# Kernel tuning notes

Hardware: AMD Instinct MI355X
Metric: run time of the kernel (lower is better)

The kernel has to match this reference:

```python
import jax, jax.numpy as jnp
import numpy as np

N, E, G = 100000, 1600000, 512
D_IN, D_H, D_OUT = 128, 128, 1
EPS = 1e-5


def _gcn_conv(x, W, b, src, dst, n):
    # PyG GCNConv: h = x @ W, add self-loops, symmetric-normalized sum aggregation, bias after.
    h = x @ W
    loop = jnp.arange(n)
    s = jnp.concatenate([src, loop])
    d = jnp.concatenate([dst, loop])
    deg = jax.ops.segment_sum(jnp.ones(s.shape[0], dtype=h.dtype), d, num_segments=n)
    dinv = jnp.where(deg > 0, jax.lax.rsqrt(deg), 0.0)
    norm = dinv[s] * dinv[d]  # [E+N]
    out = jax.ops.segment_sum(h[s] * norm[:, None], d, num_segments=n)
    return out + b


def _bn(x, g, b, m, v):
    # eval-mode BatchNorm1d
    return (x - m) * jax.lax.rsqrt(v + EPS) * g + b


def setup_inputs() -> dict:
    key = jax.random.key(0)
    ks = jax.random.split(key, 24)
    x = jax.random.normal(ks[0], (N, D_IN), dtype=jnp.float32)
    edge_index = jax.random.randint(ks[1], (2, E), 0, N, dtype=jnp.int64)
    batch = (jnp.arange(N, dtype=jnp.int64) * G) // N  # sorted, all graphs non-empty
    inp = {"x": x, "edge_index": edge_index, "batch": batch}
    dims = [(D_IN, D_H), (D_H, D_H), (D_H, D_H)]
    for i, (din, dout) in enumerate(dims):
        sc = 1.0 / np.sqrt(din)
        inp[f"W{i}"] = jax.random.normal(ks[2 + 4 * i], (din, dout), dtype=jnp.float32) * sc
        inp[f"cb{i}"] = jnp.zeros((dout,), dtype=jnp.float32)
        inp[f"g{i}"] = jnp.ones((dout,), dtype=jnp.float32)
        inp[f"bt{i}"] = jnp.zeros((dout,), dtype=jnp.float32)
        inp[f"m{i}"] = jax.random.normal(ks[3 + 4 * i], (dout,), dtype=jnp.float32) * 0.1
        inp[f"v{i}"] = jax.random.uniform(ks[4 + 4 * i], (dout,), dtype=jnp.float32, minval=0.5, maxval=1.5)
    inp["L1w"] = jax.random.normal(ks[15], (2 * D_H, D_H), dtype=jnp.float32) / np.sqrt(2 * D_H)
    inp["L1b"] = jnp.zeros((D_H,), dtype=jnp.float32)
    inp["L2w"] = jax.random.normal(ks[16], (D_H, D_H // 2), dtype=jnp.float32) / np.sqrt(D_H)
    inp["L2b"] = jnp.zeros((D_H // 2,), dtype=jnp.float32)
    inp["L3w"] = jax.random.normal(ks[17], (D_H // 2, D_OUT), dtype=jnp.float32) / np.sqrt(D_H // 2)
    inp["L3b"] = jnp.zeros((D_OUT,), dtype=jnp.float32)
    return inp


def reference(x, edge_index, batch,
              W0, cb0, g0, bt0, m0, v0,
              W1, cb1, g1, bt1, m1, v1,
              W2, cb2, g2, bt2, m2, v2,
              L1w, L1b, L2w, L2b, L3w, L3b):
    src, dst = edge_index[0], edge_index[1]
    Ws = [W0, W1, W2]
    cbs = [cb0, cb1, cb2]
    bns = [(g0, bt0, m0, v0), (g1, bt1, m1, v1), (g2, bt2, m2, v2)]
    for i in range(3):
        x_prev = x
        x = _gcn_conv(x, Ws[i], cbs[i], src, dst, N)
        x = jax.nn.relu(_bn(x, *bns[i]))
        # dropout is identity in eval mode
        if i > 0:
            x = x + x_prev  # residual (shapes match for i > 0)
    ones = jnp.ones((N,), dtype=x.dtype)
    cnt = jax.ops.segment_sum(ones, batch, num_segments=G)[:, None]
    x_mean = jax.ops.segment_sum(x, batch, num_segments=G) / cnt
    x_max = jax.ops.segment_max(x, batch, num_segments=G)
    h = jnp.concatenate([x_mean, x_max], axis=1)  # [G, 2*D_H]
    h = jax.nn.relu(h @ L1w + L1b)
    h = jax.nn.relu(h @ L2w + L2b)
    return h @ L3w + L3b  # [G, 1]
```

## Files before the change

### kernel.cpp

```cpp
#include <hip/hip_runtime.h>
#include <math.h>

#define DH 128
#define EPSB 1e-5f
#define MAXB 832
#define BCAP 2560
#define LDAP 136

typedef __attribute__((ext_vector_type(8))) short short8;
typedef __attribute__((ext_vector_type(4))) float f32x4;

static __device__ __forceinline__ unsigned short f2bf(float f) {
    unsigned u = __float_as_uint(f);
    u += 0x7fffu + ((u >> 16) & 1u);
    return (unsigned short)(u >> 16);
}
static __device__ __forceinline__ float bf2f(unsigned short h) {
    return __uint_as_float(((unsigned)h) << 16);
}
static __device__ __forceinline__ float blo(unsigned u) { return __uint_as_float(u << 16); }
static __device__ __forceinline__ float bhi(unsigned u) { return __uint_as_float(u & 0xFFFF0000u); }


__launch_bounds__(256)
__global__ void k_bucketA(const int* __restrict__ src, const int* __restrict__ dst,
                          int* __restrict__ gcur, int* __restrict__ bbuf,
                          const int* __restrict__ batch, int* __restrict__ starts,
                          const float* __restrict__ W0, const float* __restrict__ W1,
                          const float* __restrict__ W2, unsigned short* __restrict__ Wf0,
                          int E, int NB, int chunk, int N, int G)
{
    const int t = threadIdx.x;

    if (blockIdx.x >= 512) {
        int fid = (blockIdx.x - 512) * 4 + (t >> 6);
        int lane = t & 63;
        int l = fid >> 6, f = fid & 63;
        const float* W = (l == 0) ? W0 : (l == 1) ? W1 : W2;
        unsigned short* Wf = Wf0 + (size_t)l * 32768;
        int nt = f & 3, s = (f >> 2) & 3, p = (f >> 4) & 1, nh = f >> 5;
        int n = nh * 64 + nt * 16 + (lane & 15);
        int kbase = s * 32 + (lane >> 4) * 8;
        unsigned short o[8];
#pragma unroll
        for (int j = 0; j < 8; ++j) {
            float w = W[(size_t)(kbase + j) * DH + n];
            unsigned short h = f2bf(w);
            o[j] = p ? f2bf(w - bf2f(h)) : h;
        }
        unsigned short* d = Wf + (size_t)f * 512 + lane * 8;
        *(ushort4*)d       = make_ushort4(o[0], o[1], o[2], o[3]);
        *(ushort4*)(d + 4) = make_ushort4(o[4], o[5], o[6], o[7]);
        return;
    }

    __shared__ int cnt[MAXB];
    __shared__ int base[MAXB];

    for (int i = blockIdx.x * 256 + t; i < N; i += 512 * 256) {
        int b = batch[i];
        if (i == 0) { starts[0] = 0; starts[G] = N; }
        else if (batch[i - 1] != b) starts[b] = i;
    }

    for (int i = t; i < NB; i += 256) cnt[i] = 0;
    __syncthreads();
    const int e0 = blockIdx.x * chunk;
    const int e1 = min(E, e0 + chunk);
    for (int e = e0 + t; e < e1; e += 256)
        atomicAdd(&cnt[dst[e] >> 7], 1);
    __syncthreads();
    for (int i = t; i < NB; i += 256) {
        int c = cnt[i];
        base[i] = (c > 0) ? atomicAdd(&gcur[i], c) : 0;
        cnt[i] = 0;
    }
    __syncthreads();
    for (int e = e0 + t; e < e1; e += 256) {
        int d = dst[e];
        int b = d >> 7;
        int o = base[b] + atomicAdd(&cnt[b], 1);
        if (o < BCAP) bbuf[(size_t)b * BCAP + o] = (src[e] << 7) | (d & 127);
    }
}


__launch_bounds__(256)
__global__ void k_bfinal(const int* __restrict__ gcur, int* __restrict__ bbuf,
                         int2* __restrict__ rowinfo, float* __restrict__ dinv, int N)
{
    __shared__ int ebuf[BCAP];
    __shared__ int dcnt[128];
    __shared__ int sp[128];
    const int b = blockIdx.x, t = threadIdx.x;
    const int c = min(gcur[b], BCAP);
    const int base = b * BCAP;
    int* p = bbuf + base;
    for (int i = t; i < c; i += 256) ebuf[i] = p[i];
    if (t < 128) dcnt[t] = 0;
    __syncthreads();
    for (int i = t; i < c; i += 256) atomicAdd(&dcnt[ebuf[i] & 127], 1);
    __syncthreads();
    if (t < 128) sp[t] = dcnt[t];
    __syncthreads();
    for (int off = 1; off < 128; off <<= 1) {
        int u = (t < 128 && t >= off) ? sp[t - off] : 0;
        __syncthreads();
        if (t < 128) sp[t] += u;
        __syncthreads();
    }
    if (t < 128) {
        sp[t] -= dcnt[t];
        int d = b * 128 + t;
        if (d < N) {
            rowinfo[d] = make_int2(base + sp[t], base + sp[t] + dcnt[t]);
            dinv[d] = rsqrtf((float)(dcnt[t] + 1));
        }
        dcnt[t] = 0;
    }
    __syncthreads();
    for (int i = t; i < c; i += 256) {
        int e = ebuf[i];
        int dl = e & 127;
        int o = atomicAdd(&dcnt[dl], 1);
        p[sp[dl] + o] = e >> 7;
    }
}


#define LDA0 132

__launch_bounds__(256)
__global__ void k_gemm0(const float* __restrict__ X,
                        const unsigned short* __restrict__ Wf,
                        const float* __restrict__ dinv,
                        unsigned short* __restrict__ hs, int N)
{
    __shared__ float As[64 * LDA0];

    const int tid  = threadIdx.x;
    const int lane = tid & 63, wave = tid >> 6;
    const int mh = wave >> 1, nh = wave & 1;
    const int rowBase = blockIdx.x * 64;
    const int r15 = lane & 15, quad = lane >> 4;

    {
        const float4* gp = (const float4*)(X + (size_t)rowBase * DH);
#pragma unroll
        for (int it = 0; it < 8; ++it) {
            int idx = it * 256 + tid;
            int grow = idx >> 5, gcol = idx & 31;
            float4 v = make_float4(0.f, 0.f, 0.f, 0.f);
            if (rowBase + grow < N) v = gp[idx];
            *(float4*)(As + grow * LDA0 + gcol * 4) = v;
        }
    }
    __syncthreads();

    f32x4 acc[2][4];
#pragma unroll
    for (int mt = 0; mt < 2; ++mt)
#pragma unroll
        for (int nt = 0; nt < 4; ++nt)
            acc[mt][nt] = (f32x4){0.f, 0.f, 0.f, 0.f};

#pragma unroll
    for (int s = 0; s < 4; ++s) {
        short8 wfh[4], wfl[4];
#pragma unroll
        for (int nt = 0; nt < 4; ++nt) {
            wfh[nt] = *(const short8*)(Wf + ((((nh * 2 + 0) * 4 + s) * 4 + nt) * 512) + lane * 8);
            wfl[nt] = *(const short8*)(Wf + ((((nh * 2 + 1) * 4 + s) * 4 + nt) * 512) + lane * 8);
        }
#pragma unroll
        for (int mt = 0; mt < 2; ++mt) {
            const float* ap = As + (mh * 32 + mt * 16 + r15) * LDA0 + s * 32 + quad * 8;
            short8 ah, al;
#pragma unroll
            for (int j = 0; j < 8; ++j) {
                float v = ap[j];
                unsigned short h = f2bf(v);
                ah[j] = (short)h;
                al[j] = (short)f2bf(v - bf2f(h));
            }
#pragma unroll
            for (int nt = 0; nt < 4; ++nt) {
                acc[mt][nt] = __builtin_amdgcn_mfma_f32_16x16x32_bf16(ah, wfh[nt], acc[mt][nt], 0, 0, 0);
                acc[mt][nt] = __builtin_amdgcn_mfma_f32_16x16x32_bf16(ah, wfl[nt], acc[mt][nt], 0, 0, 0);
                acc[mt][nt] = __builtin_amdgcn_mfma_f32_16x16x32_bf16(al, wfh[nt], acc[mt][nt], 0, 0, 0);
            }
        }
    }

#pragma unroll
    for (int mt = 0; mt < 2; ++mt) {
        int rl = mh * 32 + mt * 16 + quad * 4;
#pragma unroll
        for (int reg = 0; reg < 4; ++reg) {
            int row = rowBase + rl + reg;
            if (row < N) {
                float sc = dinv[row];
#pragma unroll
                for (int nt = 0; nt < 4; ++nt)
                    hs[(size_t)row * DH + nh * 64 + nt * 16 + r15] = f2bf(acc[mt][nt][reg] * sc);
            }
        }
    }
}


__launch_bounds__(256)
__global__ void k_gather_mm(const unsigned short* __restrict__ hs,
                            const int2* __restrict__ rowinfo,
                            const int* __restrict__ csr_src,
                            const float* __restrict__ dinv,
                            const float* __restrict__ cb, const float* __restrict__ bm,
                            const float* __restrict__ bv, const float* __restrict__ bg,
                            const float* __restrict__ bb,
                            const float* __restrict__ prev,
                            float* __restrict__ feat,
                            const unsigned short* __restrict__ Wf,
                            unsigned short* __restrict__ hs_next,
                            int N)
{
    __shared__ unsigned short Ah[16 * LDAP];
    __shared__ unsigned short Al[16 * LDAP];

    const int tid = threadIdx.x;
    const int nb = tid >> 4, lh = tid & 15;
    const int nodeBase = blockIdx.x * 16;
    const int node = nodeBase + nb;
    const int f = lh * 8;

    if (node < N) {
        int2 ri = rowinfo[node];
        const uint4* hsv = (const uint4*)hs;
        float a[8];
        {
            uint4 sv = hsv[(size_t)node * 16 + lh];
            a[0] = blo(sv.x); a[1] = bhi(sv.x); a[2] = blo(sv.y); a[3] = bhi(sv.y);
            a[4] = blo(sv.z); a[5] = bhi(sv.z); a[6] = blo(sv.w); a[7] = bhi(sv.w);
        }
        for (int base = ri.x; base < ri.y; base += 16) {
            int cnt = ri.y - base; if (cnt > 16) cnt = 16;
            int idx = (lh < cnt) ? csr_src[base + lh] : 0;
            int i = 0;
            for (; i + 4 <= cnt; i += 4) {
                int s0 = __shfl(idx, i,     16), s1 = __shfl(idx, i + 1, 16);
                int s2 = __shfl(idx, i + 2, 16), s3 = __shfl(idx, i + 3, 16);
                uint4 v0 = hsv[(size_t)s0 * 16 + lh];
                uint4 v1 = hsv[(size_t)s1 * 16 + lh];
                uint4 v2 = hsv[(size_t)s2 * 16 + lh];
                uint4 v3 = hsv[(size_t)s3 * 16 + lh];
                a[0] += (blo(v0.x) + blo(v1.x)) + (blo(v2.x) + blo(v3.x));
                a[1] += (bhi(v0.x) + bhi(v1.x)) + (bhi(v2.x) + bhi(v3.x));
                a[2] += (blo(v0.y) + blo(v1.y)) + (blo(v2.y) + blo(v3.y));
                a[3] += (bhi(v0.y) + bhi(v1.y)) + (bhi(v2.y) + bhi(v3.y));
                a[4] += (blo(v0.z) + blo(v1.z)) + (blo(v2.z) + blo(v3.z));
                a[5] += (bhi(v0.z) + bhi(v1.z)) + (bhi(v2.z) + bhi(v3.z));
                a[6] += (blo(v0.w) + blo(v1.w)) + (blo(v2.w) + blo(v3.w));
                a[7] += (bhi(v0.w) + bhi(v1.w)) + (bhi(v2.w) + bhi(v3.w));
            }
            for (; i < cnt; ++i) {
                int s = __shfl(idx, i, 16);
                uint4 v = hsv[(size_t)s * 16 + lh];
                a[0] += blo(v.x); a[1] += bhi(v.x); a[2] += blo(v.y); a[3] += bhi(v.y);
                a[4] += blo(v.z); a[5] += bhi(v.z); a[6] += blo(v.w); a[7] += bhi(v.w);
            }
        }

        const float sc = dinv[node];
        float cbv[8], bmv[8], bvv[8], bgv[8], bbv[8];
        *(float4*)cbv = *(const float4*)(cb + f); *(float4*)(cbv + 4) = *(const float4*)(cb + f + 4);
        *(float4*)bmv = *(const float4*)(bm + f); *(float4*)(bmv + 4) = *(const float4*)(bm + f + 4);
        *(float4*)bvv = *(const float4*)(bv + f); *(float4*)(bvv + 4) = *(const float4*)(bv + f + 4);
        *(float4*)bgv = *(const float4*)(bg + f); *(float4*)(bgv + 4) = *(const float4*)(bg + f + 4);
        *(float4*)bbv = *(const float4*)(bb + f); *(float4*)(bbv + 4) = *(const float4*)(bb + f + 4);

        float o[8];
#pragma unroll
        for (int j = 0; j < 8; ++j) {
            float v = (a[j] * sc + cbv[j] - bmv[j]) * rsqrtf(bvv[j] + EPSB) * bgv[j] + bbv[j];
            o[j] = fmaxf(v, 0.f);
        }
        if (prev) {
            float4 p0 = *(const float4*)(prev + (size_t)node * DH + f);
            float4 p1 = *(const float4*)(prev + (size_t)node * DH + f + 4);
            o[0] += p0.x; o[1] += p0.y; o[2] += p0.z; o[3] += p0.w;
            o[4] += p1.x; o[5] += p1.y; o[6] += p1.z; o[7] += p1.w;
        }
        *(float4*)(feat + (size_t)node * DH + f)     = make_float4(o[0], o[1], o[2], o[3]);
        *(float4*)(feat + (size_t)node * DH + f + 4) = make_float4(o[4], o[5], o[6], o[7]);

        unsigned short hA[8], lA[8];
#pragma unroll
        for (int j = 0; j < 8; ++j) {
            unsigned short h = f2bf(o[j]);
            hA[j] = h; lA[j] = f2bf(o[j] - bf2f(h));
        }
        *(ushort4*)(Ah + nb * LDAP + f)     = make_ushort4(hA[0], hA[1], hA[2], hA[3]);
        *(ushort4*)(Ah + nb * LDAP + f + 4) = make_ushort4(hA[4], hA[5], hA[6], hA[7]);
        *(ushort4*)(Al + nb * LDAP + f)     = make_ushort4(lA[0], lA[1], lA[2], lA[3]);
        *(ushort4*)(Al + nb * LDAP + f + 4) = make_ushort4(lA[4], lA[5], lA[6], lA[7]);
    }
    __syncthreads();

    const int lane = tid & 63, wave = tid >> 6;
    const int r15 = lane & 15, quad = lane >> 4;

    f32x4 acc[2];
    acc[0] = (f32x4){0.f, 0.f, 0.f, 0.f};
    acc[1] = (f32x4){0.f, 0.f, 0.f, 0.f};

#pragma unroll
    for (int s = 0; s < 4; ++s) {
        short8 ah = *(const short8*)(Ah + r15 * LDAP + s * 32 + quad * 8);
        short8 al = *(const short8*)(Al + r15 * LDAP + s * 32 + quad * 8);
#pragma unroll
        for (int j = 0; j < 2; ++j) {
            int ntg = wave * 2 + j;
            int nh = ntg >> 2, nt = ntg & 3;
            short8 wh = *(const short8*)(Wf + ((((nh * 2 + 0) * 4 + s) * 4 + nt) * 512) + lane * 8);
            short8 wl = *(const short8*)(Wf + ((((nh * 2 + 1) * 4 + s) * 4 + nt) * 512) + lane * 8);
            acc[j] = __builtin_amdgcn_mfma_f32_16x16x32_bf16(ah, wh, acc[j], 0, 0, 0);
            acc[j] = __builtin_amdgcn_mfma_f32_16x16x32_bf16(ah, wl, acc[j], 0, 0, 0);
            acc[j] = __builtin_amdgcn_mfma_f32_16x16x32_bf16(al, wh, acc[j], 0, 0, 0);
        }
    }

    float dv[4];
#pragma unroll
    for (int reg = 0; reg < 4; ++reg) {
        int row = nodeBase + quad * 4 + reg;
        dv[reg] = (row < N) ? dinv[row] : 0.f;
    }
#pragma unroll
    for (int j = 0; j < 2; ++j) {
        int col = (wave * 2 + j) * 16 + r15;
#pragma unroll
        for (int reg = 0; reg < 4; ++reg) {
            int row = nodeBase + quad * 4 + reg;
            if (row < N)
                hs_next[(size_t)row * DH + col] = f2bf(acc[j][reg] * dv[reg]);
        }
    }
}


__launch_bounds__(256)
__global__ void k_gather_fin(const unsigned short* __restrict__ hs,
                             const int2* __restrict__ rowinfo,
                             const int* __restrict__ csr_src,
                             const float* __restrict__ dinv,
                             const float* __restrict__ cb, const float* __restrict__ bm,
                             const float* __restrict__ bv, const float* __restrict__ bg,
                             const float* __restrict__ bb,
                             const float* __restrict__ prev,
                             float* __restrict__ feat, int N)
{
    const int node = (blockIdx.x * blockDim.x + threadIdx.x) >> 4;
    const int lh = threadIdx.x & 15;
    if (node >= N) return;
    const int f = lh * 8;
    int2 ri = rowinfo[node];

    const uint4* hsv = (const uint4*)hs;
    float a[8];
    {
        uint4 sv = hsv[(size_t)node * 16 + lh];
        a[0] = blo(sv.x); a[1] = bhi(sv.x); a[2] = blo(sv.y); a[3] = bhi(sv.y);
        a[4] = blo(sv.z); a[5] = bhi(sv.z); a[6] = blo(sv.w); a[7] = bhi(sv.w);
    }
    for (int base = ri.x; base < ri.y; base += 16) {
        int cnt = ri.y - base; if (cnt > 16) cnt = 16;
        int idx = (lh < cnt) ? csr_src[base + lh] : 0;
        int i = 0;
        for (; i + 4 <= cnt; i += 4) {
            int s0 = __shfl(idx, i,     16), s1 = __shfl(idx, i + 1, 16);
            int s2 = __shfl(idx, i + 2, 16), s3 = __shfl(idx, i + 3, 16);
            uint4 v0 = hsv[(size_t)s0 * 16 + lh];
            uint4 v1 = hsv[(size_t)s1 * 16 + lh];
            uint4 v2 = hsv[(size_t)s2 * 16 + lh];
            uint4 v3 = hsv[(size_t)s3 * 16 + lh];
            a[0] += (blo(v0.x) + blo(v1.x)) + (blo(v2.x) + blo(v3.x));
            a[1] += (bhi(v0.x) + bhi(v1.x)) + (bhi(v2.x) + bhi(v3.x));
            a[2] += (blo(v0.y) + blo(v1.y)) + (blo(v2.y) + blo(v3.y));
            a[3] += (bhi(v0.y) + bhi(v1.y)) + (bhi(v2.y) + bhi(v3.y));
            a[4] += (blo(v0.z) + blo(v1.z)) + (blo(v2.z) + blo(v3.z));
            a[5] += (bhi(v0.z) + bhi(v1.z)) + (bhi(v2.z) + bhi(v3.z));
            a[6] += (blo(v0.w) + blo(v1.w)) + (blo(v2.w) + blo(v3.w));
            a[7] += (bhi(v0.w) + bhi(v1.w)) + (bhi(v2.w) + bhi(v3.w));
        }
        for (; i < cnt; ++i) {
            int s = __shfl(idx, i, 16);
            uint4 v = hsv[(size_t)s * 16 + lh];
            a[0] += blo(v.x); a[1] += bhi(v.x); a[2] += blo(v.y); a[3] += bhi(v.y);
            a[4] += blo(v.z); a[5] += bhi(v.z); a[6] += blo(v.w); a[7] += bhi(v.w);
        }
    }

    const float sc = dinv[node];
    float cbv[8], bmv[8], bvv[8], bgv[8], bbv[8];
    *(float4*)cbv = *(const float4*)(cb + f); *(float4*)(cbv + 4) = *(const float4*)(cb + f + 4);
    *(float4*)bmv = *(const float4*)(bm + f); *(float4*)(bmv + 4) = *(const float4*)(bm + f + 4);
    *(float4*)bvv = *(const float4*)(bv + f); *(float4*)(bvv + 4) = *(const float4*)(bv + f + 4);
    *(float4*)bgv = *(const float4*)(bg + f); *(float4*)(bgv + 4) = *(const float4*)(bg + f + 4);
    *(float4*)bbv = *(const float4*)(bb + f); *(float4*)(bbv + 4) = *(const float4*)(bb + f + 4);

    float4 p0 = *(const float4*)(prev + (size_t)node * DH + f);
    float4 p1 = *(const float4*)(prev + (size_t)node * DH + f + 4);
    float o[8];
#pragma unroll
    for (int j = 0; j < 8; ++j) {
        float v = (a[j] * sc + cbv[j] - bmv[j]) * rsqrtf(bvv[j] + EPSB) * bgv[j] + bbv[j];
        o[j] = fmaxf(v, 0.f);
    }
    o[0] += p0.x; o[1] += p0.y; o[2] += p0.z; o[3] += p0.w;
    o[4] += p1.x; o[5] += p1.y; o[6] += p1.z; o[7] += p1.w;

    *(float4*)(feat + (size_t)node * DH + f)     = make_float4(o[0], o[1], o[2], o[3]);
    *(float4*)(feat + (size_t)node * DH + f + 4) = make_float4(o[4], o[5], o[6], o[7]);
}


__launch_bounds__(256)
__global__ void k_pool_mlp(const float* __restrict__ x, const int* __restrict__ starts,
                           const float* __restrict__ L1w, const float* __restrict__ L1b,
                           const float* __restrict__ L2w, const float* __restrict__ L2b,
                           const float* __restrict__ L3w, const float* __restrict__ L3b,
                           float* __restrict__ out)
{
    int g = blockIdx.x, t = threadIdx.x;
    int s0 = starts[g], s1 = starts[g + 1];
    const int rg = t >> 6;
    const int tc = t & 63;
    const int fc = tc * 2;

    float sA = 0.f, sB = 0.f;
    float mA = -INFINITY, mB = -INFINITY;
    for (int i = s0 + rg; i < s1; i += 4) {
        float2 v = *(const float2*)(x + (size_t)i * DH + fc);
        sA += v.x; sB += v.y;
        mA = fmaxf(mA, v.x); mB = fmaxf(mB, v.y);
    }

    __shared__ float ps[4][128];
    __shared__ float pm[4][128];
    ps[rg][fc] = sA; ps[rg][fc + 1] = sB;
    pm[rg][fc] = mA; pm[rg][fc + 1] = mB;
    __syncthreads();

    __shared__ float h[256];
    if (rg == 0) {
        float inv = 1.f / (float)(s1 - s0);
#pragma unroll
        for (int j = 0; j < 2; ++j) {
            int fi = fc + j;
            h[fi] = ((ps[0][fi] + ps[1][fi]) + (ps[2][fi] + ps[3][fi])) * inv;
            h[128 + fi] = fmaxf(fmaxf(pm[0][fi], pm[1][fi]), fmaxf(pm[2][fi], pm[3][fi]));
        }
    }
    __syncthreads();

    __shared__ float h1[128];
    if (t < 128) {
        float a = L1b[t];
        for (int k = 0; k < 256; ++k) a += h[k] * L1w[k * DH + t];
        h1[t] = fmaxf(a, 0.f);
    }
    __syncthreads();

    __shared__ float h2[64];
    if (t < 64) {
        float a2 = L2b[t];
        for (int k = 0; k < 128; ++k) a2 += h1[k] * L2w[k * 64 + t];
        h2[t] = fmaxf(a2, 0.f);
    }
    __syncthreads();

    if (t < 64) {
        float p = h2[t] * L3w[t];
#pragma unroll
        for (int off = 32; off > 0; off >>= 1) p += __shfl_down(p, off, 64);
        if (t == 0) out[g] = p + L3b[0];
    }
}


static inline char* align16(char* p) {
    return (char*)(((uintptr_t)p + 15) & ~(uintptr_t)15);
}

extern "C" void kernel_launch(void* const* d_in, const int* in_sizes, int n_in,
                              void* d_out, int out_size, void* d_ws, size_t ws_size,
                              hipStream_t stream)
{
    const float* x     = (const float*)d_in[0];
    const int*   ei    = (const int*)d_in[1];
    const int*   batch = (const int*)d_in[2];
    const int N = in_sizes[0] / DH;
    const int E = in_sizes[1] / 2;
    const int G = out_size;
    const int* src = ei;
    const int* dst = ei + E;

    const float* W[3]  = {(const float*)d_in[3],  (const float*)d_in[9],  (const float*)d_in[15]};
    const float* cb[3] = {(const float*)d_in[4],  (const float*)d_in[10], (const float*)d_in[16]};
    const float* bg[3] = {(const float*)d_in[5],  (const float*)d_in[11], (const float*)d_in[17]};
    const float* bt[3] = {(const float*)d_in[6],  (const float*)d_in[12], (const float*)d_in[18]};
    const float* bm[3] = {(const float*)d_in[7],  (const float*)d_in[13], (const float*)d_in[19]};
    const float* bv[3] = {(const float*)d_in[8],  (const float*)d_in[14], (const float*)d_in[20]};
    const float* L1w = (const float*)d_in[21]; const float* L1b = (const float*)d_in[22];
    const float* L2w = (const float*)d_in[23]; const float* L2b = (const float*)d_in[24];
    const float* L3w = (const float*)d_in[25]; const float* L3b = (const float*)d_in[26];

    char* wsp = (char*)d_ws;
    size_t featB = (size_t)N * DH * sizeof(float);
    size_t hsB   = (size_t)N * DH * sizeof(unsigned short);
    float* F_A = (float*)wsp; wsp += featB;
    float* F_B = (float*)wsp; wsp += featB;
    unsigned short* HS0 = (unsigned short*)F_B;
    unsigned short* HS1 = (unsigned short*)wsp; wsp += hsB;
    unsigned short* HS2 = (unsigned short*)wsp; wsp += hsB;
    unsigned short* Wfrag = (unsigned short*)wsp; wsp += 3 * 65536;
    int2*  rowinfo = (int2*)wsp;  wsp += (size_t)N * sizeof(int2);
    float* dinv    = (float*)wsp; wsp += (size_t)N * sizeof(float);
    int*   starts  = (int*)wsp;   wsp = align16(wsp + (size_t)(G + 1) * sizeof(int));
    int*   gcur    = (int*)wsp;   wsp = align16(wsp + (size_t)MAXB * sizeof(int));
    int*   bbuf    = (int*)wsp;   wsp += (size_t)MAXB * BCAP * sizeof(int);

    const int NB = (N + 127) >> 7;
    const int nblkA = 512;
    const int chunk = (E + nblkA - 1) / nblkA;

    hipMemsetAsync(gcur, 0, (size_t)NB * sizeof(int), stream);
    k_bucketA<<<nblkA + 48, 256, 0, stream>>>(src, dst, gcur, bbuf, batch, starts,
                                              W[0], W[1], W[2], Wfrag,
                                              E, NB, chunk, N, G);
    k_bfinal <<<NB, 256, 0, stream>>>(gcur, bbuf, rowinfo, dinv, N);

    int gemmGrid = (N + 63) / 64;
    int gathGrid = ((size_t)N * 16 + 255) / 256;

    k_gemm0<<<gemmGrid, 256, 0, stream>>>(x, Wfrag, dinv, HS0, N);
    k_gather_mm<<<gathGrid, 256, 0, stream>>>(HS0, rowinfo, bbuf, dinv,
                                              cb[0], bm[0], bv[0], bg[0], bt[0],
                                              nullptr, F_A, Wfrag + 32768, HS1, N);
    k_gather_mm<<<gathGrid, 256, 0, stream>>>(HS1, rowinfo, bbuf, dinv,
                                              cb[1], bm[1], bv[1], bg[1], bt[1],
                                              F_A, F_B, Wfrag + 65536, HS2, N);
    k_gather_fin<<<gathGrid, 256, 0, stream>>>(HS2, rowinfo, bbuf, dinv,
                                               cb[2], bm[2], bv[2], bg[2], bt[2],
                                               F_B, F_B, N);

    k_pool_mlp<<<G, 256, 0, stream>>>(F_B, starts, L1w, L1b, L2w, L2b, L3w, L3b,
                                      (float*)d_out);
}
```

Baseline: 486.7 us.

## Fuse last GCN layer with graph pooling; pre-split bf16 input tiles in gemm0

The final gather kernel now accumulates per-graph sum and max directly. It uses shared-memory atomics per block, then global atomics. This removes the write and re-read of the full last-layer feature matrix and the separate pooling pass, leaving only a small MLP head kernel. The float max relies on unsigned-integer atomicMax over nonnegative activations starting from zero. In the first GEMM, the hi/lo bf16 split of the input is done once at load time into MFMA-fragment-ordered LDS, instead of being recomputed by each wave. The trade-off is atomic contention and the assumption that each 16-node block spans at most two graphs.

```diff
diff --git a/kernel.cpp b/kernel.cpp
--- a/kernel.cpp
+++ b/kernel.cpp
@@ -128,15 +128,14 @@
 }
 
 
-#define LDA0 132
-
 __launch_bounds__(256)
 __global__ void k_gemm0(const float* __restrict__ X,
                         const unsigned short* __restrict__ Wf,
                         const float* __restrict__ dinv,
                         unsigned short* __restrict__ hs, int N)
 {
-    __shared__ float As[64 * LDA0];
+    __shared__ unsigned short Ah[16 * 512];
+    __shared__ unsigned short Al[16 * 512];
 
     const int tid  = threadIdx.x;
     const int lane = tid & 63, wave = tid >> 6;
@@ -145,14 +144,35 @@
     const int r15 = lane & 15, quad = lane >> 4;
 
     {
-        const float4* gp = (const float4*)(X + (size_t)rowBase * DH);
-#pragma unroll
-        for (int it = 0; it < 8; ++it) {
-            int idx = it * 256 + tid;
-            int grow = idx >> 5, gcol = idx & 31;
-            float4 v = make_float4(0.f, 0.f, 0.f, 0.f);
-            if (rowBase + grow < N) v = gp[idx];
-            *(float4*)(As + grow * LDA0 + gcol * 4) = v;
+        const int gl = tid >> 4;
+        const int f8 = (tid & 15) * 8;
+        const int s  = f8 >> 5;
+        const int q  = (f8 >> 3) & 3;
+        const int lp = q * 16 + gl;
+#pragma unroll
+        for (int it = 0; it < 4; ++it) {
+            int row = rowBase + it * 16 + gl;
+            float v[8];
+            if (row < N) {
+                float4 a0 = *(const float4*)(X + (size_t)row * DH + f8);
+                float4 a1 = *(const float4*)(X + (size_t)row * DH + f8 + 4);
+                v[0] = a0.x; v[1] = a0.y; v[2] = a0.z; v[3] = a0.w;
+                v[4] = a1.x; v[5] = a1.y; v[6] = a1.z; v[7] = a1.w;
+            } else {
+#pragma unroll
+                for (int j = 0; j < 8; ++j) v[j] = 0.f;
+            }
+            unsigned short hA[8], lA[8];
+#pragma unroll
+            for (int j = 0; j < 8; ++j) {
+                unsigned short h = f2bf(v[j]);
+                hA[j] = h; lA[j] = f2bf(v[j] - bf2f(h));
+            }
+            int reg = it * 4 + s;
+            *(ushort4*)(Ah + reg * 512 + lp * 8)     = make_ushort4(hA[0], hA[1], hA[2], hA[3]);
+            *(ushort4*)(Ah + reg * 512 + lp * 8 + 4) = make_ushort4(hA[4], hA[5], hA[6], hA[7]);
+            *(ushort4*)(Al + reg * 512 + lp * 8)     = make_ushort4(lA[0], lA[1], lA[2], lA[3]);
+            *(ushort4*)(Al + reg * 512 + lp * 8 + 4) = make_ushort4(lA[4], lA[5], lA[6], lA[7]);
         }
     }
     __syncthreads();
@@ -174,15 +194,9 @@
         }
 #pragma unroll
         for (int mt = 0; mt < 2; ++mt) {
-            const float* ap = As + (mh * 32 + mt * 16 + r15) * LDA0 + s * 32 + quad * 8;
-            short8 ah, al;
-#pragma unroll
-            for (int j = 0; j < 8; ++j) {
-                float v = ap[j];
-                unsigned short h = f2bf(v);
-                ah[j] = (short)h;
-                al[j] = (short)f2bf(v - bf2f(h));
-            }
+            int reg = (mh * 2 + mt) * 4 + s;
+            short8 ah = *(const short8*)(Ah + reg * 512 + lane * 8);
+            short8 al = *(const short8*)(Al + reg * 512 + lane * 8);
 #pragma unroll
             for (int nt = 0; nt < 4; ++nt) {
                 acc[mt][nt] = __builtin_amdgcn_mfma_f32_16x16x32_bf16(ah, wfh[nt], acc[mt][nt], 0, 0, 0);
@@ -348,126 +362,131 @@
 
 
 __launch_bounds__(256)
-__global__ void k_gather_fin(const unsigned short* __restrict__ hs,
-                             const int2* __restrict__ rowinfo,
-                             const int* __restrict__ csr_src,
-                             const float* __restrict__ dinv,
-                             const float* __restrict__ cb, const float* __restrict__ bm,
-                             const float* __restrict__ bv, const float* __restrict__ bg,
-                             const float* __restrict__ bb,
-                             const float* __restrict__ prev,
-                             float* __restrict__ feat, int N)
-{
-    const int node = (blockIdx.x * blockDim.x + threadIdx.x) >> 4;
-    const int lh = threadIdx.x & 15;
-    if (node >= N) return;
+__global__ void k_gather_pool(const unsigned short* __restrict__ hs,
+                              const int2* __restrict__ rowinfo,
+                              const int* __restrict__ csr_src,
+                              const float* __restrict__ dinv,
+                              const float* __restrict__ cb, const float* __restrict__ bm,
+                              const float* __restrict__ bv, const float* __restrict__ bg,
+                              const float* __restrict__ bb,
+                              const float* __restrict__ prev,
+                              const int* __restrict__ batch,
+                              float* __restrict__ sumAcc,
+                              unsigned* __restrict__ maxAcc,
+                              int N)
+{
+    __shared__ float    ssum[256];
+    __shared__ unsigned smax[256];
+
+    const int tid = threadIdx.x;
+    const int nb = tid >> 4, lh = tid & 15;
+    const int nodeBase = blockIdx.x * 16;
+    const int node = nodeBase + nb;
     const int f = lh * 8;
-    int2 ri = rowinfo[node];
-
-    const uint4* hsv = (const uint4*)hs;
-    float a[8];
-    {
-        uint4 sv = hsv[(size_t)node * 16 + lh];
-        a[0] = blo(sv.x); a[1] = bhi(sv.x); a[2] = blo(sv.y); a[3] = bhi(sv.y);
-        a[4] = blo(sv.z); a[5] = bhi(sv.z); a[6] = blo(sv.w); a[7] = bhi(sv.w);
-    }
-    for (int base = ri.x; base < ri.y; base += 16) {
-        int cnt = ri.y - base; if (cnt > 16) cnt = 16;
-        int idx = (lh < cnt) ? csr_src[base + lh] : 0;
-        int i = 0;
-        for (; i + 4 <= cnt; i += 4) {
-            int s0 = __shfl(idx, i,     16), s1 = __shfl(idx, i + 1, 16);
-            int s2 = __shfl(idx, i + 2, 16), s3 = __shfl(idx, i + 3, 16);
-            uint4 v0 = hsv[(size_t)s0 * 16 + lh];
-            uint4 v1 = hsv[(size_t)s1 * 16 + lh];
-            uint4 v2 = hsv[(size_t)s2 * 16 + lh];
-            uint4 v3 = hsv[(size_t)s3 * 16 + lh];
-            a[0] += (blo(v0.x) + blo(v1.x)) + (blo(v2.x) + blo(v3.x));
-            a[1] += (bhi(v0.x) + bhi(v1.x)) + (bhi(v2.x) + bhi(v3.x));
-            a[2] += (blo(v0.y) + blo(v1.y)) + (blo(v2.y) + blo(v3.y));
-            a[3] += (bhi(v0.y) + bhi(v1.y)) + (bhi(v2.y) + bhi(v3.y));
-            a[4] += (blo(v0.z) + blo(v1.z)) + (blo(v2.z) + blo(v3.z));
-            a[5] += (bhi(v0.z) + bhi(v1.z)) + (bhi(v2.z) + bhi(v3.z));
-            a[6] += (blo(v0.w) + blo(v1.w)) + (blo(v2.w) + blo(v3.w));
-            a[7] += (bhi(v0.w) + bhi(v1.w)) + (bhi(v2.w) + bhi(v3.w));
-        }
-        for (; i < cnt; ++i) {
-            int s = __shfl(idx, i, 16);
-            uint4 v = hsv[(size_t)s * 16 + lh];
-            a[0] += blo(v.x); a[1] += bhi(v.x); a[2] += blo(v.y); a[3] += bhi(v.y);
-            a[4] += blo(v.z); a[5] += bhi(v.z); a[6] += blo(v.w); a[7] += bhi(v.w);
-        }
-    }
-
-    const float sc = dinv[node];
-    float cbv[8], bmv[8], bvv[8], bgv[8], bbv[8];
-    *(float4*)cbv = *(const float4*)(cb + f); *(float4*)(cbv + 4) = *(const float4*)(cb + f + 4);
-    *(float4*)bmv = *(const float4*)(bm + f); *(float4*)(bmv + 4) = *(const float4*)(bm + f + 4);
-    *(float4*)bvv = *(const float4*)(bv + f); *(float4*)(bvv + 4) = *(const float4*)(bv + f + 4);
-    *(float4*)bgv = *(const float4*)(bg + f); *(float4*)(bgv + 4) = *(const float4*)(bg + f + 4);
-    *(float4*)bbv = *(const float4*)(bb + f); *(float4*)(bbv + 4) = *(const float4*)(bb + f + 4);
-
-    float4 p0 = *(const float4*)(prev + (size_t)node * DH + f);
-    float4 p1 = *(const float4*)(prev + (size_t)node * DH + f + 4);
-    float o[8];
-#pragma unroll
-    for (int j = 0; j < 8; ++j) {
-        float v = (a[j] * sc + cbv[j] - bmv[j]) * rsqrtf(bvv[j] + EPSB) * bgv[j] + bbv[j];
-        o[j] = fmaxf(v, 0.f);
-    }
-    o[0] += p0.x; o[1] += p0.y; o[2] += p0.z; o[3] += p0.w;
-    o[4] += p1.x; o[5] += p1.y; o[6] += p1.z; o[7] += p1.w;
-
-    *(float4*)(feat + (size_t)node * DH + f)     = make_float4(o[0], o[1], o[2], o[3]);
-    *(float4*)(feat + (size_t)node * DH + f + 4) = make_float4(o[4], o[5], o[6], o[7]);
-}
-
-
-__launch_bounds__(256)
-__global__ void k_pool_mlp(const float* __restrict__ x, const int* __restrict__ starts,
-                           const float* __restrict__ L1w, const float* __restrict__ L1b,
-                           const float* __restrict__ L2w, const float* __restrict__ L2b,
-                           const float* __restrict__ L3w, const float* __restrict__ L3b,
-                           float* __restrict__ out)
+
+    const int g0 = batch[nodeBase];
+    const int g1 = batch[min(nodeBase + 15, N - 1)];
+
+    ssum[tid] = 0.f;
+    smax[tid] = 0u;
+    __syncthreads();
+
+    if (node < N) {
+        int2 ri = rowinfo[node];
+        const uint4* hsv = (const uint4*)hs;
+        float a[8];
+        {
+            uint4 sv = hsv[(size_t)node * 16 + lh];
+            a[0] = blo(sv.x); a[1] = bhi(sv.x); a[2] = blo(sv.y); a[3] = bhi(sv.y);
+            a[4] = blo(sv.z); a[5] = bhi(sv.z); a[6] = blo(sv.w); a[7] = bhi(sv.w);
+        }
+        for (int base = ri.x; base < ri.y; base += 16) {
+            int cnt = ri.y - base; if (cnt > 16) cnt = 16;
+            int idx = (lh < cnt) ? csr_src[base + lh] : 0;
+            int i = 0;
+            for (; i + 4 <= cnt; i += 4) {
+                int s0 = __shfl(idx, i,     16), s1 = __shfl(idx, i + 1, 16);
+                int s2 = __shfl(idx, i + 2, 16), s3 = __shfl(idx, i + 3, 16);
+                uint4 v0 = hsv[(size_t)s0 * 16 + lh];
+                uint4 v1 = hsv[(size_t)s1 * 16 + lh];
+                uint4 v2 = hsv[(size_t)s2 * 16 + lh];
+                uint4 v3 = hsv[(size_t)s3 * 16 + lh];
+                a[0] += (blo(v0.x) + blo(v1.x)) + (blo(v2.x) + blo(v3.x));
+                a[1] += (bhi(v0.x) + bhi(v1.x)) + (bhi(v2.x) + bhi(v3.x));
+                a[2] += (blo(v0.y) + blo(v1.y)) + (blo(v2.y) + blo(v3.y));
+                a[3] += (bhi(v0.y) + bhi(v1.y)) + (bhi(v2.y) + bhi(v3.y));
+                a[4] += (blo(v0.z) + blo(v1.z)) + (blo(v2.z) + blo(v3.z));
+                a[5] += (bhi(v0.z) + bhi(v1.z)) + (bhi(v2.z) + bhi(v3.z));
+                a[6] += (blo(v0.w) + blo(v1.w)) + (blo(v2.w) + blo(v3.w));
+                a[7] += (bhi(v0.w) + bhi(v1.w)) + (bhi(v2.w) + bhi(v3.w));
+            }
+            for (; i < cnt; ++i) {
+                int s = __shfl(idx, i, 16);
+                uint4 v = hsv[(size_t)s * 16 + lh];
+                a[0] += blo(v.x); a[1] += bhi(v.x); a[2] += blo(v.y); a[3] += bhi(v.y);
+                a[4] += blo(v.z); a[5] += bhi(v.z); a[6] += blo(v.w); a[7] += bhi(v.w);
+            }
+        }
+
+        const float sc = dinv[node];
+        float cbv[8], bmv[8], bvv[8], bgv[8], bbv[8];
+        *(float4*)cbv = *(const float4*)(cb + f); *(float4*)(cbv + 4) = *(const float4*)(cb + f + 4);
+        *(float4*)bmv = *(const float4*)(bm + f); *(float4*)(bmv + 4) = *(const float4*)(bm + f + 4);
+        *(float4*)bvv = *(const float4*)(bv + f); *(float4*)(bvv + 4) = *(const float4*)(bv + f + 4);
+        *(float4*)bgv = *(const float4*)(bg + f); *(float4*)(bgv + 4) = *(const float4*)(bg + f + 4);
+        *(float4*)bbv = *(const float4*)(bb + f); *(float4*)(bbv + 4) = *(const float4*)(bb + f + 4);
+
+        float4 p0 = *(const float4*)(prev + (size_t)node * DH + f);
+        float4 p1 = *(const float4*)(prev + (size_t)node * DH + f + 4);
+        float o[8];
+#pragma unroll
+        for (int j = 0; j < 8; ++j) {
+            float v = (a[j] * sc + cbv[j] - bmv[j]) * rsqrtf(bvv[j] + EPSB) * bgv[j] + bbv[j];
+            o[j] = fmaxf(v, 0.f);
+        }
+        o[0] += p0.x; o[1] += p0.y; o[2] += p0.z; o[3] += p0.w;
+        o[4] += p1.x; o[5] += p1.y; o[6] += p1.z; o[7] += p1.w;
+
+        const int seg = (batch[node] != g0) ? 1 : 0;
+        float*    sp = ssum + seg * 128 + f;
+        unsigned* mp = smax + seg * 128 + f;
+#pragma unroll
+        for (int j = 0; j < 8; ++j) {
+            atomicAdd(&sp[j], o[j]);
+            atomicMax(&mp[j], __float_as_uint(o[j]));
+        }
+    }
+    __syncthreads();
+
+    const int seg = tid >> 7, fi = tid & 127;
+    if (seg == 0 || g1 != g0) {
+        int g = g0 + seg;
+        atomicAdd(&sumAcc[(size_t)g * 128 + fi], ssum[tid]);
+        atomicMax(&maxAcc[(size_t)g * 128 + fi], smax[tid]);
+    }
+}
+
+
+__launch_bounds__(128)
+__global__ void k_head(const float* __restrict__ sumAcc, const unsigned* __restrict__ maxAcc,
+                       const int* __restrict__ starts,
+                       const float* __restrict__ L1w, const float* __restrict__ L1b,
+                       const float* __restrict__ L2w, const float* __restrict__ L2b,
+                       const float* __restrict__ L3w, const float* __restrict__ L3b,
+                       float* __restrict__ out)
 {
     int g = blockIdx.x, t = threadIdx.x;
-    int s0 = starts[g], s1 = starts[g + 1];
-    const int rg = t >> 6;
-    const int tc = t & 63;
-    const int fc = tc * 2;
-
-    float sA = 0.f, sB = 0.f;
-    float mA = -INFINITY, mB = -INFINITY;
-    for (int i = s0 + rg; i < s1; i += 4) {
-        float2 v = *(const float2*)(x + (size_t)i * DH + fc);
-        sA += v.x; sB += v.y;
-        mA = fmaxf(mA, v.x); mB = fmaxf(mB, v.y);
-    }
-
-    __shared__ float ps[4][128];
-    __shared__ float pm[4][128];
-    ps[rg][fc] = sA; ps[rg][fc + 1] = sB;
-    pm[rg][fc] = mA; pm[rg][fc + 1] = mB;
-    __syncthreads();
+    float cnt = (float)(starts[g + 1] - starts[g]);
 
     __shared__ float h[256];
-    if (rg == 0) {
-        float inv = 1.f / (float)(s1 - s0);
-#pragma unroll
-        for (int j = 0; j < 2; ++j) {
-            int fi = fc + j;
-            h[fi] = ((ps[0][fi] + ps[1][fi]) + (ps[2][fi] + ps[3][fi])) * inv;
-            h[128 + fi] = fmaxf(fmaxf(pm[0][fi], pm[1][fi]), fmaxf(pm[2][fi], pm[3][fi]));
-        }
-    }
-    __syncthreads();
-
+    h[t]       = sumAcc[(size_t)g * 128 + t] / cnt;
+    h[128 + t] = __uint_as_float(maxAcc[(size_t)g * 128 + t]);
+    __syncthreads();
+
+    float a = L1b[t];
+    for (int k = 0; k < 256; ++k) a += h[k] * L1w[k * DH + t];
     __shared__ float h1[128];
-    if (t < 128) {
-        float a = L1b[t];
-        for (int k = 0; k < 256; ++k) a += h[k] * L1w[k * DH + t];
-        h1[t] = fmaxf(a, 0.f);
-    }
+    h1[t] = fmaxf(a, 0.f);
     __syncthreads();
 
     __shared__ float h2[64];
@@ -526,21 +545,24 @@
     int2*  rowinfo = (int2*)wsp;  wsp += (size_t)N * sizeof(int2);
     float* dinv    = (float*)wsp; wsp += (size_t)N * sizeof(float);
     int*   starts  = (int*)wsp;   wsp = align16(wsp + (size_t)(G + 1) * sizeof(int));
-    int*   gcur    = (int*)wsp;   wsp = align16(wsp + (size_t)MAXB * sizeof(int));
-    int*   bbuf    = (int*)wsp;   wsp += (size_t)MAXB * BCAP * sizeof(int);
+    int*      gcur   = (int*)wsp;      wsp += (size_t)MAXB * sizeof(int);
+    float*    sumAcc = (float*)wsp;    wsp += (size_t)G * 128 * sizeof(float);
+    unsigned* maxAcc = (unsigned*)wsp; wsp += (size_t)G * 128 * sizeof(unsigned);
+    size_t zeroBytes = (size_t)MAXB * sizeof(int) + (size_t)G * 128 * 8;
+    int*   bbuf    = (int*)align16(wsp); wsp = (char*)bbuf + (size_t)MAXB * BCAP * sizeof(int);
 
     const int NB = (N + 127) >> 7;
     const int nblkA = 512;
     const int chunk = (E + nblkA - 1) / nblkA;
 
-    hipMemsetAsync(gcur, 0, (size_t)NB * sizeof(int), stream);
+    hipMemsetAsync(gcur, 0, zeroBytes, stream);
     k_bucketA<<<nblkA + 48, 256, 0, stream>>>(src, dst, gcur, bbuf, batch, starts,
                                               W[0], W[1], W[2], Wfrag,
                                               E, NB, chunk, N, G);
     k_bfinal <<<NB, 256, 0, stream>>>(gcur, bbuf, rowinfo, dinv, N);
 
     int gemmGrid = (N + 63) / 64;
-    int gathGrid = ((size_t)N * 16 + 255) / 256;
+    int gathGrid = (N + 15) / 16;
 
     k_gemm0<<<gemmGrid, 256, 0, stream>>>(x, Wfrag, dinv, HS0, N);
     k_gather_mm<<<gathGrid, 256, 0, stream>>>(HS0, rowinfo, bbuf, dinv,
@@ -549,10 +571,10 @@
     k_gather_mm<<<gathGrid, 256, 0, stream>>>(HS1, rowinfo, bbuf, dinv,
                                               cb[1], bm[1], bv[1], bg[1], bt[1],
                                               F_A, F_B, Wfrag + 65536, HS2, N);
-    k_gather_fin<<<gathGrid, 256, 0, stream>>>(HS2, rowinfo, bbuf, dinv,
-                                               cb[2], bm[2], bv[2], bg[2], bt[2],
-                                               F_B, F_B, N);
-
-    k_pool_mlp<<<G, 256, 0, stream>>>(F_B, starts, L1w, L1b, L2w, L2b, L3w, L3b,
-                                      (float*)d_out);
-}
+    k_gather_pool<<<gathGrid, 256, 0, stream>>>(HS2, rowinfo, bbuf, dinv,
+                                                cb[2], bm[2], bv[2], bg[2], bt[2],
+                                                F_B, batch, sumAcc, maxAcc, N);
+
+    k_head<<<G, 128, 0, stream>>>(sumAcc, maxAcc, starts,
+                                  L1w, L1b, L2w, L2b, L3w, L3b, (float*)d_out);
+}
```

New measurement: 500.8 us. 2.9% more time.
